# Kernel tuning notes

Measured on AMD Instinct MI355X. Metric: run time of the kernel, lower is better.

Reference implementation:

```python
import jax, jax.numpy as jnp
import numpy as np

D_MODEL = 1024
NUM_HEADS = 16
GROUPS = 4
HEADS_PER_GROUP = NUM_HEADS // GROUPS
D_K = D_MODEL // NUM_HEADS
B, S = 2, 2048


def setup_inputs() -> dict:
    key = jax.random.key(0)
    ks = jax.random.split(key, 10)
    sc = 0.02
    return {
        "x": jax.random.normal(ks[0], (B, S, D_MODEL), dtype=jnp.float32),
        "W_Q": jax.random.normal(ks[1], (D_MODEL, D_MODEL), dtype=jnp.float32) * sc,
        "b_Q": jnp.zeros((D_MODEL,), dtype=jnp.float32),
        "W_K": jax.random.normal(ks[2], (GROUPS, D_MODEL, D_K), dtype=jnp.float32) * sc,
        "b_K": jnp.zeros((GROUPS, D_K), dtype=jnp.float32),
        "W_V": jax.random.normal(ks[3], (GROUPS, D_MODEL, D_K), dtype=jnp.float32) * sc,
        "b_V": jnp.zeros((GROUPS, D_K), dtype=jnp.float32),
        "W_O": jax.random.normal(ks[4], (D_MODEL, D_MODEL), dtype=jnp.float32) * sc,
        "b_O": jnp.zeros((D_MODEL,), dtype=jnp.float32),
    }


def reference(x, W_Q, b_Q, W_K, b_K, W_V, b_V, W_O, b_O):
    b, s, _ = x.shape
    # Q: [b, s, d_model] -> [b, groups, heads_per_group, s, d_k]
    Q = (x @ W_Q + b_Q).reshape(b, s, NUM_HEADS, D_K).transpose(0, 2, 1, 3)
    Q = Q.reshape(b, GROUPS, HEADS_PER_GROUP, s, D_K)
    # Shared K/V per group: [b, groups, s, d_k]
    K = jnp.einsum('bsd,gdk->bgsk', x, W_K) + b_K[None, :, None, :]
    V = jnp.einsum('bsd,gdk->bgsk', x, W_V) + b_V[None, :, None, :]
    # scores: [b, groups, heads_per_group, s, s]
    scores = jnp.einsum('bghsk,bgtk->bghst', Q, K) / jnp.sqrt(jnp.float32(D_K))
    attn = jax.nn.softmax(scores, axis=-1)
    # context: [b, groups, heads_per_group, s, d_k] -> [b, s, d_model]
    ctx = jnp.einsum('bghst,bgtk->bghsk', attn, V)
    ctx = ctx.reshape(b, NUM_HEADS, s, D_K).transpose(0, 2, 1, 3).reshape(b, s, D_MODEL)
    return ctx @ W_O + b_O
```

## Files before the change

### kernel.cpp

```cpp
#include <hip/hip_runtime.h>
#include <cstdint>
#include <cstddef>

typedef short bf16x8 __attribute__((ext_vector_type(8)));
typedef float f32x4 __attribute__((ext_vector_type(4)));

#define DM 1024
#define NHEADS 16
#define NGROUPS 4
#define DK 64
#define BATCH 2
#define SEQ 2048
#define MROWS 4096

#define QB_ELEMS   ((size_t)BATCH*NHEADS*SEQ*DK)
#define KB_ELEMS   ((size_t)BATCH*NGROUPS*SEQ*DK)
#define VT_ELEMS   KB_ELEMS
#define XC_ELEMS   ((size_t)MROWS*DM)
#define WQKV_ELEMS ((size_t)1536*DM)
#define WO_ELEMS   ((size_t)DM*DM)

#define SCL_Q 0.180336880f

__device__ __forceinline__ ushort f2bf(float f) {
    union { float f; uint32_t u; } a; a.f = f;
    uint32_t u = a.u;
    return (ushort)((u + 0x7FFFu + ((u >> 16) & 1u)) >> 16);
}

__device__ __forceinline__ void gll16(const void* g, void* l) {
    __builtin_amdgcn_global_load_lds((const __attribute__((address_space(1))) void*)g,
                                     (__attribute__((address_space(3))) void*)l, 16, 0, 0);
}

__device__ __forceinline__ void transpose_tile(
        const float* __restrict__ src, int src_ld, ushort* __restrict__ dst,
        int r0, int c0, int tid, float (*tl)[65])
{
    const int rr = tid >> 4, cc = (tid & 15) * 4;
#pragma unroll
    for (int p = 0; p < 4; p++) {
        int r = rr + p * 16;
        float4 v = *(const float4*)(src + (size_t)(r0 + r) * src_ld + c0 + cc);
        tl[cc + 0][r] = v.x; tl[cc + 1][r] = v.y;
        tl[cc + 2][r] = v.z; tl[cc + 3][r] = v.w;
    }
    __syncthreads();
#pragma unroll
    for (int p = 0; p < 4; p++) {
        int c = rr + p * 16;
        ushort4 o;
        o.x = f2bf(tl[c][cc + 0]); o.y = f2bf(tl[c][cc + 1]);
        o.z = f2bf(tl[c][cc + 2]); o.w = f2bf(tl[c][cc + 3]);
        *(ushort4*)(dst + (size_t)(c0 + c) * 1024 + r0 + cc) = o;
    }
}

__global__ __launch_bounds__(256) void gqa_prep_kernel(
        const float* __restrict__ x,
        const float* __restrict__ WQ, const float* __restrict__ WK,
        const float* __restrict__ WV,
        const float* __restrict__ bQ, const float* __restrict__ bK,
        const float* __restrict__ bV,
        ushort* __restrict__ xbf, ushort* __restrict__ WqkvT,
        float* __restrict__ bcat)
{
    __shared__ float tl[64][65];
    const int bid = blockIdx.x, tid = threadIdx.x;
    if (bid < 256) {
        transpose_tile(WQ, 1024, WqkvT, (bid >> 4) * 64, (bid & 15) * 64, tid, tl);
    } else if (bid < 320) {
        int t = bid - 256, g = t >> 4;
        transpose_tile(WK + (size_t)g * 1024 * 64, 64,
                       WqkvT + (size_t)(1024 + g * 64) * 1024,
                       (t & 15) * 64, 0, tid, tl);
    } else if (bid < 384) {
        int t = bid - 320, g = t >> 4;
        transpose_tile(WV + (size_t)g * 1024 * 64, 64,
                       WqkvT + (size_t)(1280 + g * 64) * 1024,
                       (t & 15) * 64, 0, tid, tl);
    } else if (bid < 640) {
        int cid = bid - 384;
        const float* xs = x + (size_t)cid * 16384;
        ushort* xd = xbf + (size_t)cid * 16384;
#pragma unroll
        for (int p = 0; p < 16; p++) {
            float4 v = *(const float4*)(xs + p * 1024 + tid * 4);
            ushort4 o = { f2bf(v.x), f2bf(v.y), f2bf(v.z), f2bf(v.w) };
            *(ushort4*)(xd + p * 1024 + tid * 4) = o;
        }
    } else {
        for (int i = tid; i < 1536; i += 256) {
            float v = (i < 1024) ? bQ[i] : (i < 1280 ? bK[i - 1024] : bV[i - 1280]);
            bcat[i] = v;
        }
    }
}

template<int BN>
__global__ __launch_bounds__(256, 2) void gqa_qkv_kernel(
        const ushort* __restrict__ A, const ushort* __restrict__ BT,
        const float* __restrict__ bias,
        ushort* __restrict__ Qb, ushort* __restrict__ Kb, ushort* __restrict__ Vtg,
        const float* __restrict__ WO, ushort* __restrict__ WoT)
{
    __shared__ ushort smem[4][8192];
    const int tid = threadIdx.x;
    int i = blockIdx.x;

    if (i < 256) {
        float (*tl)[65] = (float(*)[65])&smem[0][0];
        transpose_tile(WO, 1024, WoT, (i >> 4) * 64, (i & 15) * 64, tid, tl);
        return;
    }
    i -= 256;

    const int xcd = i & 7, slot = i >> 3;
    const int bm = (slot / BN) * 8 + xcd;
    const int bn = slot % BN;
    const int wave = tid >> 6, lane = tid & 63;
    const int wm = (wave & 1) * 64, wn = (wave >> 1) * 64;
    const int lr = lane & 15, lq = lane >> 4;
    const int swz = lr & 7;

    const ushort* srcA[4]; const ushort* srcB[4]; int dstOff[4];
#pragma unroll
    for (int p = 0; p < 4; p++) {
        int slt = p * 256 + tid;
        int row = slt >> 3, cb = (slt & 7) ^ (row & 7);
        srcA[p] = A  + (size_t)(bm * 128 + row) * 1024 + cb * 8;
        srcB[p] = BT + (size_t)(bn * 128 + row) * 1024 + cb * 8;
        dstOff[p] = p * 2048 + wave * 512;
    }

    f32x4 acc[4][4];
#pragma unroll
    for (int ii = 0; ii < 4; ii++)
#pragma unroll
        for (int j = 0; j < 4; j++) acc[ii][j] = (f32x4){0.f, 0.f, 0.f, 0.f};

#pragma unroll
    for (int p = 0; p < 4; p++) {
        gll16(srcA[p], &smem[0][dstOff[p]]);
        gll16(srcB[p], &smem[2][dstOff[p]]);
    }

    for (int kt = 0; kt < 16; kt++) {
        __syncthreads();
        if (kt < 15) {
            int buf = (kt + 1) & 1, ko = (kt + 1) * 64;
#pragma unroll
            for (int p = 0; p < 4; p++) {
                gll16(srcA[p] + ko, &smem[buf][dstOff[p]]);
                gll16(srcB[p] + ko, &smem[2 + buf][dstOff[p]]);
            }
        }
        const ushort* as = smem[kt & 1];
        const ushort* bs = smem[2 + (kt & 1)];
        bf16x8 af[2][4], bfr[2][4];
#pragma unroll
        for (int kh = 0; kh < 2; kh++) {
#pragma unroll
            for (int ii = 0; ii < 4; ii++)
                af[kh][ii] = *(const bf16x8*)&as[(wm + ii * 16 + lr) * 64 + ((kh * 4 + lq) ^ swz) * 8];
#pragma unroll
            for (int j = 0; j < 4; j++)
                bfr[kh][j] = *(const bf16x8*)&bs[(wn + j * 16 + lr) * 64 + ((kh * 4 + lq) ^ swz) * 8];
        }
#pragma unroll
        for (int kh = 0; kh < 2; kh++)
#pragma unroll
            for (int ii = 0; ii < 4; ii++)
#pragma unroll
                for (int j = 0; j < 4; j++)
                    acc[ii][j] = __builtin_amdgcn_mfma_f32_16x16x32_bf16(af[kh][ii], bfr[kh][j], acc[ii][j], 0, 0, 0);
    }

#pragma unroll
    for (int ii = 0; ii < 4; ii++) {
        int mg = bm * 128 + wm + ii * 16 + lq * 4;
        int b = mg >> 11, s = mg & 2047;
#pragma unroll
        for (int j = 0; j < 4; j++) {
            int cg = bn * 128 + wn + j * 16 + lr;
            float bv = bias[cg];
            int d = cg & 63;
            if (cg < 1024) {
                int h = cg >> 6;
                ushort* dst = Qb + ((size_t)(b * NHEADS + h) * SEQ + s) * DK + d;
#pragma unroll
                for (int r = 0; r < 4; r++)
                    dst[r * DK] = f2bf((acc[ii][j][r] + bv) * SCL_Q);
            } else if (cg < 1280) {
                int g = (cg - 1024) >> 6;
                ushort* dst = Kb + ((size_t)(b * NGROUPS + g) * SEQ + s) * DK + d;
#pragma unroll
                for (int r = 0; r < 4; r++) dst[r * DK] = f2bf(acc[ii][j][r] + bv);
            } else {
                int g = (cg - 1280) >> 6;
                int s4 = s >> 2, kg = s4 & 7;
                int col = ((s4 >> 3) << 5) + (((((kg & 3) << 1) | (kg >> 2))) << 2);
                ushort4 pk;
                pk.x = f2bf(acc[ii][j][0] + bv); pk.y = f2bf(acc[ii][j][1] + bv);
                pk.z = f2bf(acc[ii][j][2] + bv); pk.w = f2bf(acc[ii][j][3] + bv);
                *(ushort4*)(Vtg + ((size_t)(b * NGROUPS + g) * DK + d) * SEQ + col) = pk;
            }
        }
    }
}

__global__ __launch_bounds__(256, 2) void gqa_oproj_kernel(
        const ushort* __restrict__ A, const ushort* __restrict__ BT,
        const float* __restrict__ bias, float* __restrict__ outF)
{
    constexpr int NJ = 2;
    constexpr int BNT = NJ * 32;
    __shared__ ushort smem[16384 + NJ * 4096];
    ushort* As = smem;
    ushort* Bs = smem + 16384;

    const int tid = threadIdx.x;
    const int i = blockIdx.x;
    const int xcd = i & 7, slot = i >> 3;
    const int bm = (slot >> 4) * 8 + xcd;
    const int bn = slot & 15;
    const int wave = tid >> 6, lane = tid & 63;
    const int wm = (wave & 1) * 64, wn = (wave >> 1) * (NJ * 16);
    const int lr = lane & 15, lq = lane >> 4;
    const int swz = lr & 7;

    const ushort* srcA[4]; int dstOffA[4];
    const ushort* srcB[NJ]; int dstOffB[NJ];
#pragma unroll
    for (int p = 0; p < 4; p++) {
        int slt = p * 256 + tid;
        int row = slt >> 3, cb = (slt & 7) ^ (row & 7);
        srcA[p] = A + (size_t)(bm * 128 + row) * 1024 + cb * 8;
        dstOffA[p] = p * 2048 + wave * 512;
    }
#pragma unroll
    for (int p = 0; p < NJ; p++) {
        int slt = p * 256 + tid;
        int row = slt >> 3, cb = (slt & 7) ^ (row & 7);
        srcB[p] = BT + (size_t)(bn * BNT + row) * 1024 + cb * 8;
        dstOffB[p] = p * 2048 + wave * 512;
    }

    f32x4 acc[4][NJ];
#pragma unroll
    for (int ii = 0; ii < 4; ii++)
#pragma unroll
        for (int j = 0; j < NJ; j++) acc[ii][j] = (f32x4){0.f, 0.f, 0.f, 0.f};

#pragma unroll
    for (int p = 0; p < 4; p++) gll16(srcA[p], &As[dstOffA[p]]);
#pragma unroll
    for (int p = 0; p < NJ; p++) gll16(srcB[p], &Bs[dstOffB[p]]);

    for (int kt = 0; kt < 16; kt++) {
        __syncthreads();
        if (kt < 15) {
            int buf = (kt + 1) & 1, ko = (kt + 1) * 64;
#pragma unroll
            for (int p = 0; p < 4; p++)
                gll16(srcA[p] + ko, &As[buf * 8192 + dstOffA[p]]);
#pragma unroll
            for (int p = 0; p < NJ; p++)
                gll16(srcB[p] + ko, &Bs[buf * (NJ * 2048) + dstOffB[p]]);
        }
        const ushort* as = As + (kt & 1) * 8192;
        const ushort* bs = Bs + (kt & 1) * (NJ * 2048);
        bf16x8 af[2][4], bfr[2][NJ];
#pragma unroll
        for (int kh = 0; kh < 2; kh++) {
#pragma unroll
            for (int ii = 0; ii < 4; ii++)
                af[kh][ii] = *(const bf16x8*)&as[(wm + ii * 16 + lr) * 64 + ((kh * 4 + lq) ^ swz) * 8];
#pragma unroll
            for (int j = 0; j < NJ; j++)
                bfr[kh][j] = *(const bf16x8*)&bs[(wn + j * 16 + lr) * 64 + ((kh * 4 + lq) ^ swz) * 8];
        }
#pragma unroll
        for (int kh = 0; kh < 2; kh++)
#pragma unroll
            for (int ii = 0; ii < 4; ii++)
#pragma unroll
                for (int j = 0; j < NJ; j++)
                    acc[ii][j] = __builtin_amdgcn_mfma_f32_16x16x32_bf16(af[kh][ii], bfr[kh][j], acc[ii][j], 0, 0, 0);
    }

#pragma unroll
    for (int ii = 0; ii < 4; ii++) {
        int mg = bm * 128 + wm + ii * 16 + lq * 4;
#pragma unroll
        for (int j = 0; j < NJ; j++) {
            int cg = bn * BNT + wn + j * 16 + lr;
            float bv = bias[cg];
#pragma unroll
            for (int r = 0; r < 4; r++)
                outF[(size_t)(mg + r) * DM + cg] = acc[ii][j][r] + bv;
        }
    }
}

__global__ __launch_bounds__(256, 2) void gqa_attn_kernel(
        const ushort* __restrict__ Qb, const ushort* __restrict__ Kb,
        const ushort* __restrict__ Vtg, ushort* __restrict__ ctx)
{
    __shared__ ushort Ks[2][128 * 64];
    __shared__ ushort Vs[2][64 * 128];

    const int tid = threadIdx.x, wave = tid >> 6, lane = tid & 63;
    const int lr = lane & 15, lq = lane >> 4;
    const int swz = lr & 7;
    const int wq = wave & 1, wt = wave >> 1;
    const int i = blockIdx.x;
    const int bg = i & 7, s2 = i >> 3;
    const int qt = s2 & 15, h = s2 >> 4;
    const int b = bg >> 2, g = bg & 3, hg = g * 4 + h;

    const ushort* Qh = Qb  + (size_t)(b * NHEADS  + hg) * SEQ * DK;
    const ushort* Kg = Kb  + (size_t)(b * NGROUPS + g)  * SEQ * DK;
    const ushort* Vg = Vtg + (size_t)(b * NGROUPS + g)  * DK * SEQ;

    const int s0 = qt * 128 + wq * 64;
    const int tb = wt * 64;

    bf16x8 qf[4][2];
#pragma unroll
    for (int qs = 0; qs < 4; qs++)
#pragma unroll
        for (int kh = 0; kh < 2; kh++)
            qf[qs][kh] = *(const bf16x8*)(Qh + (size_t)(s0 + qs * 16 + lr) * DK + kh * 32 + lq * 8);

    const ushort* srcK[4]; const ushort* srcV[4]; int dstOff[4];
#pragma unroll
    for (int p = 0; p < 4; p++) {
        int slt = p * 256 + tid;
        int krow = slt >> 3, kcb = (slt & 7) ^ (krow & 7);
        srcK[p] = Kg + (size_t)krow * DK + kcb * 8;
        int vrow = slt >> 4, vc = slt & 15;
        int vcb = (vc & 8) | ((vc ^ vrow) & 7);
        srcV[p] = Vg + (size_t)vrow * SEQ + vcb * 8;
        dstOff[p] = (p * 256 + wave * 64) * 8;
    }

    f32x4 of[4][4];
#pragma unroll
    for (int qs = 0; qs < 4; qs++)
#pragma unroll
        for (int j = 0; j < 4; j++) of[qs][j] = (f32x4){0.f, 0.f, 0.f, 0.f};
    f32x4 accL[4];
#pragma unroll
    for (int qs = 0; qs < 4; qs++) accL[qs] = (f32x4){0.f, 0.f, 0.f, 0.f};

    bf16x8 ones;
#pragma unroll
    for (int k = 0; k < 8; k++) ones[k] = (short)0x3F80;

#pragma unroll
    for (int p = 0; p < 4; p++) {
        gll16(srcK[p], &Ks[0][dstOff[p]]);
        gll16(srcV[p], &Vs[0][dstOff[p]]);
    }

    for (int it = 0; it < 16; it++) {
        __syncthreads();
        if (it < 15) {
            int buf = (it + 1) & 1, t0 = (it + 1) * 128;
#pragma unroll
            for (int p = 0; p < 4; p++) {
                gll16(srcK[p] + (size_t)t0 * DK, &Ks[buf][dstOff[p]]);
                gll16(srcV[p] + t0, &Vs[buf][dstOff[p]]);
            }
        }
        const ushort* ks = Ks[it & 1];
        const ushort* vs = Vs[it & 1];

        bf16x8 kf[4][2];
#pragma unroll
        for (int nt = 0; nt < 4; nt++)
#pragma unroll
            for (int kh = 0; kh < 2; kh++)
                kf[nt][kh] = *(const bf16x8*)&ks[(tb + nt * 16 + lr) * 64 + ((kh * 4 + lq) ^ swz) * 8];

        bf16x8 vf[4][2];
#pragma unroll
        for (int j = 0; j < 4; j++)
#pragma unroll
            for (int kk = 0; kk < 2; kk++)
                vf[j][kk] = *(const bf16x8*)&vs[(j * 16 + lr) * 128 + (wt * 8 + ((kk * 4 + lq) ^ swz)) * 8];

        f32x4 sc[4][4];
#pragma unroll
        for (int qs = 0; qs < 4; qs++)
#pragma unroll
            for (int nt = 0; nt < 4; nt++) {
                f32x4 s = (f32x4){0.f, 0.f, 0.f, 0.f};
                s = __builtin_amdgcn_mfma_f32_16x16x32_bf16(kf[nt][0], qf[qs][0], s, 0, 0, 0);
                s = __builtin_amdgcn_mfma_f32_16x16x32_bf16(kf[nt][1], qf[qs][1], s, 0, 0, 0);
                sc[qs][nt] = s;
            }

        union PF { bf16x8 v; uint32_t w[4]; };
        PF pf[4][2];
#pragma unroll
        for (int qs = 0; qs < 4; qs++) {
#pragma unroll
            for (int nt = 0; nt < 4; nt++) {
                union { float f; uint32_t u; } e0, e1, e2, e3;
                e0.f = __builtin_amdgcn_exp2f(sc[qs][nt][0]);
                e1.f = __builtin_amdgcn_exp2f(sc[qs][nt][1]);
                e2.f = __builtin_amdgcn_exp2f(sc[qs][nt][2]);
                e3.f = __builtin_amdgcn_exp2f(sc[qs][nt][3]);
                pf[qs][nt >> 1].w[(nt & 1) * 2 + 0] = __builtin_amdgcn_perm(e1.u, e0.u, 0x07060302u);
                pf[qs][nt >> 1].w[(nt & 1) * 2 + 1] = __builtin_amdgcn_perm(e3.u, e2.u, 0x07060302u);
            }
            accL[qs] = __builtin_amdgcn_mfma_f32_16x16x32_bf16(ones, pf[qs][0].v, accL[qs], 0, 0, 0);
            accL[qs] = __builtin_amdgcn_mfma_f32_16x16x32_bf16(ones, pf[qs][1].v, accL[qs], 0, 0, 0);
        }

#pragma unroll
        for (int qs = 0; qs < 4; qs++)
#pragma unroll
            for (int j = 0; j < 4; j++) {
                of[qs][j] = __builtin_amdgcn_mfma_f32_16x16x32_bf16(vf[j][0], pf[qs][0].v, of[qs][j], 0, 0, 0);
                of[qs][j] = __builtin_amdgcn_mfma_f32_16x16x32_bf16(vf[j][1], pf[qs][1].v, of[qs][j], 0, 0, 0);
            }
    }

    __syncthreads();
    float* comb = (float*)&Ks[0][0];
    float* accX = (float*)&Vs[0][0];
    if (wt == 1) {
        float* cw = comb + wq * 4096;
#pragma unroll
        for (int qs = 0; qs < 4; qs++)
#pragma unroll
            for (int j = 0; j < 4; j++)
                *(f32x4*)&cw[(qs * 4 + j) * 256 + lane * 4] = of[qs][j];
        if (lq == 0) {
#pragma unroll
            for (int qs = 0; qs < 4; qs++) accX[(wq * 4 + qs) * 16 + lr] = accL[qs][0];
        }
    }
    __syncthreads();
    if (wt == 0) {
        const float* cw = comb + wq * 4096;
        float inv[4];
#pragma unroll
        for (int qs = 0; qs < 4; qs++)
            inv[qs] = 1.0f / (accL[qs][0] + accX[(wq * 4 + qs) * 16 + lr]);
        ushort* cbp = ctx + (size_t)b * SEQ * DM;
#pragma unroll
        for (int qs = 0; qs < 4; qs++) {
            int s = s0 + qs * 16 + lr;
#pragma unroll
            for (int j = 0; j < 4; j++) {
                f32x4 o2 = of[qs][j] + *(const f32x4*)&cw[(qs * 4 + j) * 256 + lane * 4];
                ushort4 o;
                o.x = f2bf(o2[0] * inv[qs]);
                o.y = f2bf(o2[1] * inv[qs]);
                o.z = f2bf(o2[2] * inv[qs]);
                o.w = f2bf(o2[3] * inv[qs]);
                *(ushort4*)(cbp + (size_t)s * DM + hg * 64 + j * 16 + lq * 4) = o;
            }
        }
    }
}

extern "C" void kernel_launch(void* const* d_in, const int* in_sizes, int n_in,
                              void* d_out, int out_size, void* d_ws, size_t ws_size,
                              hipStream_t stream) {
    const float* x  = (const float*)d_in[0];
    const float* WQ = (const float*)d_in[1];
    const float* bQ = (const float*)d_in[2];
    const float* WK = (const float*)d_in[3];
    const float* bK = (const float*)d_in[4];
    const float* WV = (const float*)d_in[5];
    const float* bV = (const float*)d_in[6];
    const float* WO = (const float*)d_in[7];
    const float* bO = (const float*)d_in[8];

    ushort* Qb    = (ushort*)d_ws;
    ushort* Kb    = Qb + QB_ELEMS;
    ushort* Vtg   = Kb + KB_ELEMS;
    ushort* xc    = Vtg + VT_ELEMS;
    ushort* WqkvT = xc + XC_ELEMS;
    ushort* WoT   = WqkvT + WQKV_ELEMS;
    float*  bcat  = (float*)(WoT + WO_ELEMS);

    gqa_prep_kernel<<<641, 256, 0, stream>>>(x, WQ, WK, WV, bQ, bK, bV,
                                             xc, WqkvT, bcat);
    gqa_qkv_kernel<12><<<640, 256, 0, stream>>>(
        xc, WqkvT, bcat, Qb, Kb, Vtg, WO, WoT);
    gqa_attn_kernel<<<512, 256, 0, stream>>>(Qb, Kb, Vtg, xc);
    gqa_oproj_kernel<<<512, 256, 0, stream>>>(xc, WoT, bO, (float*)d_out);
}
```

Before: 157.1 us.

## Halve attention KV tile to 64 keys, raise occupancy, add MFMA priority hints

The attention kernel now streams K/V in 64-key tiles instead of 128, halving the shared-memory buffers and per-iteration register fragments, and raises launch bounds from 2 to 4 blocks per CU. This is meant to hide memory and softmax latency through more resident waves. It also wraps MFMA phases in s_setprio to favour matrix issue, and moves the row-sum exchange into its own small shared array. In exchange there are twice as many loop iterations and barriers, and a tighter register budget that may cause spills.

```diff
diff --git a/kernel.cpp b/kernel.cpp
--- a/kernel.cpp
+++ b/kernel.cpp
@@ -303,12 +303,13 @@
     }
 }
 
-__global__ __launch_bounds__(256, 2) void gqa_attn_kernel(
+__global__ __launch_bounds__(256, 4) void gqa_attn_kernel(
         const ushort* __restrict__ Qb, const ushort* __restrict__ Kb,
         const ushort* __restrict__ Vtg, ushort* __restrict__ ctx)
 {
-    __shared__ ushort Ks[2][128 * 64];
-    __shared__ ushort Vs[2][64 * 128];
+    __shared__ ushort Ks[2][64 * 64];
+    __shared__ ushort Vs[2][64 * 64];
+    __shared__ float accXs[128];
 
     const int tid = threadIdx.x, wave = tid >> 6, lane = tid & 63;
     const int lr = lane & 15, lq = lane >> 4;
@@ -324,7 +325,7 @@
     const ushort* Vg = Vtg + (size_t)(b * NGROUPS + g)  * DK * SEQ;
 
     const int s0 = qt * 128 + wq * 64;
-    const int tb = wt * 64;
+    const int tb = wt * 32;
 
     bf16x8 qf[4][2];
 #pragma unroll
@@ -333,14 +334,14 @@
         for (int kh = 0; kh < 2; kh++)
             qf[qs][kh] = *(const bf16x8*)(Qh + (size_t)(s0 + qs * 16 + lr) * DK + kh * 32 + lq * 8);
 
-    const ushort* srcK[4]; const ushort* srcV[4]; int dstOff[4];
-#pragma unroll
-    for (int p = 0; p < 4; p++) {
+    const ushort* srcK[2]; const ushort* srcV[2]; int dstOff[2];
+#pragma unroll
+    for (int p = 0; p < 2; p++) {
         int slt = p * 256 + tid;
         int krow = slt >> 3, kcb = (slt & 7) ^ (krow & 7);
         srcK[p] = Kg + (size_t)krow * DK + kcb * 8;
-        int vrow = slt >> 4, vc = slt & 15;
-        int vcb = (vc & 8) | ((vc ^ vrow) & 7);
+        int vrow = slt >> 3, vc = slt & 7;
+        int vcb = (vc ^ vrow) & 7;
         srcV[p] = Vg + (size_t)vrow * SEQ + vcb * 8;
         dstOff[p] = (p * 256 + wave * 64) * 8;
     }
@@ -359,17 +360,17 @@
     for (int k = 0; k < 8; k++) ones[k] = (short)0x3F80;
 
 #pragma unroll
-    for (int p = 0; p < 4; p++) {
+    for (int p = 0; p < 2; p++) {
         gll16(srcK[p], &Ks[0][dstOff[p]]);
         gll16(srcV[p], &Vs[0][dstOff[p]]);
     }
 
-    for (int it = 0; it < 16; it++) {
+    for (int it = 0; it < 32; it++) {
         __syncthreads();
-        if (it < 15) {
-            int buf = (it + 1) & 1, t0 = (it + 1) * 128;
-#pragma unroll
-            for (int p = 0; p < 4; p++) {
+        if (it < 31) {
+            int buf = (it + 1) & 1, t0 = (it + 1) * 64;
+#pragma unroll
+            for (int p = 0; p < 2; p++) {
                 gll16(srcK[p] + (size_t)t0 * DK, &Ks[buf][dstOff[p]]);
                 gll16(srcV[p] + t0, &Vs[buf][dstOff[p]]);
             }
@@ -377,63 +378,65 @@
         const ushort* ks = Ks[it & 1];
         const ushort* vs = Vs[it & 1];
 
-        bf16x8 kf[4][2];
-#pragma unroll
-        for (int nt = 0; nt < 4; nt++)
+        bf16x8 kf[2][2];
+#pragma unroll
+        for (int nt = 0; nt < 2; nt++)
 #pragma unroll
             for (int kh = 0; kh < 2; kh++)
                 kf[nt][kh] = *(const bf16x8*)&ks[(tb + nt * 16 + lr) * 64 + ((kh * 4 + lq) ^ swz) * 8];
 
-        bf16x8 vf[4][2];
-#pragma unroll
-        for (int j = 0; j < 4; j++)
-#pragma unroll
-            for (int kk = 0; kk < 2; kk++)
-                vf[j][kk] = *(const bf16x8*)&vs[(j * 16 + lr) * 128 + (wt * 8 + ((kk * 4 + lq) ^ swz)) * 8];
-
-        f32x4 sc[4][4];
+        bf16x8 vf[4];
+        {
+            int gch = wt * 4 + lq;
+            int vc2 = (gch ^ swz) & 7;
+#pragma unroll
+            for (int j = 0; j < 4; j++)
+                vf[j] = *(const bf16x8*)&vs[(j * 16 + lr) * 64 + vc2 * 8];
+        }
+
+        f32x4 sc[4][2];
+        __builtin_amdgcn_s_setprio(1);
 #pragma unroll
         for (int qs = 0; qs < 4; qs++)
 #pragma unroll
-            for (int nt = 0; nt < 4; nt++) {
+            for (int nt = 0; nt < 2; nt++) {
                 f32x4 s = (f32x4){0.f, 0.f, 0.f, 0.f};
                 s = __builtin_amdgcn_mfma_f32_16x16x32_bf16(kf[nt][0], qf[qs][0], s, 0, 0, 0);
                 s = __builtin_amdgcn_mfma_f32_16x16x32_bf16(kf[nt][1], qf[qs][1], s, 0, 0, 0);
                 sc[qs][nt] = s;
             }
+        __builtin_amdgcn_s_setprio(0);
 
         union PF { bf16x8 v; uint32_t w[4]; };
-        PF pf[4][2];
-#pragma unroll
-        for (int qs = 0; qs < 4; qs++) {
-#pragma unroll
-            for (int nt = 0; nt < 4; nt++) {
+        PF pf[4];
+#pragma unroll
+        for (int qs = 0; qs < 4; qs++)
+#pragma unroll
+            for (int nt = 0; nt < 2; nt++) {
                 union { float f; uint32_t u; } e0, e1, e2, e3;
                 e0.f = __builtin_amdgcn_exp2f(sc[qs][nt][0]);
                 e1.f = __builtin_amdgcn_exp2f(sc[qs][nt][1]);
                 e2.f = __builtin_amdgcn_exp2f(sc[qs][nt][2]);
                 e3.f = __builtin_amdgcn_exp2f(sc[qs][nt][3]);
-                pf[qs][nt >> 1].w[(nt & 1) * 2 + 0] = __builtin_amdgcn_perm(e1.u, e0.u, 0x07060302u);
-                pf[qs][nt >> 1].w[(nt & 1) * 2 + 1] = __builtin_amdgcn_perm(e3.u, e2.u, 0x07060302u);
+                pf[qs].w[nt * 2 + 0] = __builtin_amdgcn_perm(e1.u, e0.u, 0x07060302u);
+                pf[qs].w[nt * 2 + 1] = __builtin_amdgcn_perm(e3.u, e2.u, 0x07060302u);
             }
-            accL[qs] = __builtin_amdgcn_mfma_f32_16x16x32_bf16(ones, pf[qs][0].v, accL[qs], 0, 0, 0);
-            accL[qs] = __builtin_amdgcn_mfma_f32_16x16x32_bf16(ones, pf[qs][1].v, accL[qs], 0, 0, 0);
-        }
-
+
+        __builtin_amdgcn_s_setprio(1);
 #pragma unroll
         for (int qs = 0; qs < 4; qs++)
-#pragma unroll
-            for (int j = 0; j < 4; j++) {
-                of[qs][j] = __builtin_amdgcn_mfma_f32_16x16x32_bf16(vf[j][0], pf[qs][0].v, of[qs][j], 0, 0, 0);
-                of[qs][j] = __builtin_amdgcn_mfma_f32_16x16x32_bf16(vf[j][1], pf[qs][1].v, of[qs][j], 0, 0, 0);
-            }
+            accL[qs] = __builtin_amdgcn_mfma_f32_16x16x32_bf16(ones, pf[qs].v, accL[qs], 0, 0, 0);
+#pragma unroll
+        for (int qs = 0; qs < 4; qs++)
+#pragma unroll
+            for (int j = 0; j < 4; j++)
+                of[qs][j] = __builtin_amdgcn_mfma_f32_16x16x32_bf16(vf[j], pf[qs].v, of[qs][j], 0, 0, 0);
+        __builtin_amdgcn_s_setprio(0);
     }
 
     __syncthreads();
-    float* comb = (float*)&Ks[0][0];
-    float* accX = (float*)&Vs[0][0];
+    float* cw = (wq == 0) ? (float*)&Ks[0][0] : (float*)&Vs[0][0];
     if (wt == 1) {
-        float* cw = comb + wq * 4096;
 #pragma unroll
         for (int qs = 0; qs < 4; qs++)
 #pragma unroll
@@ -441,16 +444,15 @@
                 *(f32x4*)&cw[(qs * 4 + j) * 256 + lane * 4] = of[qs][j];
         if (lq == 0) {
 #pragma unroll
-            for (int qs = 0; qs < 4; qs++) accX[(wq * 4 + qs) * 16 + lr] = accL[qs][0];
+            for (int qs = 0; qs < 4; qs++) accXs[(wq * 4 + qs) * 16 + lr] = accL[qs][0];
         }
     }
     __syncthreads();
     if (wt == 0) {
-        const float* cw = comb + wq * 4096;
         float inv[4];
 #pragma unroll
         for (int qs = 0; qs < 4; qs++)
-            inv[qs] = 1.0f / (accL[qs][0] + accX[(wq * 4 + qs) * 16 + lr]);
+            inv[qs] = 1.0f / (accL[qs][0] + accXs[(wq * 4 + qs) * 16 + lr]);
         ushort* cbp = ctx + (size_t)b * SEQ * DM;
 #pragma unroll
         for (int qs = 0; qs < 4; qs++) {
```

Measured after the change: 323.6 us. 2.06x slower.
